# Kernel optimization log

Hardware: AMD Instinct MI355X
Metric: run time of the kernel (lower is better)

Reference implementation:

```python
import jax, jax.numpy as jnp
import numpy as np

GROUP = 32  # values per quantization group (per-group scale)

def setup_inputs() -> dict:
    key = jax.random.key(0)
    k1, k2, k3, k4 = jax.random.split(key, 4)
    B, S, IN, OUT = 4, 2048, 4096, 4096
    x = jax.random.normal(k1, (B, S, IN), dtype=jnp.float32)
    # packed 4-bit weights: each int32 byte-value in [0,256) holds two nibbles
    w_packed = jax.random.randint(k2, (OUT, IN // 2), 0, 256, dtype=jnp.int32)
    scales = jax.random.uniform(k3, (OUT, IN // GROUP), dtype=jnp.float32) * 0.02 + 0.001
    bias = jax.random.normal(k4, (OUT,), dtype=jnp.float32)
    return {"x": x, "w_packed": w_packed, "scales": scales, "bias": bias}

def _dequantize(w_packed, scales):
    # w_packed: [OUT, IN//2] int32 bytes, scales: [OUT, IN//GROUP]
    OUT = w_packed.shape[0]
    low = w_packed & 0xF
    high = (w_packed >> 4) & 0xF
    q = jnp.stack([low, high], axis=-1).reshape(OUT, -1)  # [OUT, IN]
    qf = q.astype(jnp.float32) - 8.0  # signed 4-bit centered at 8
    qg = qf.reshape(OUT, scales.shape[1], GROUP)
    w = qg * scales[:, :, None]
    return w.reshape(OUT, -1)  # [OUT, IN]

def reference(x, w_packed, scales, bias):
    # dequantize weights then F.linear: y = x @ W^T + b
    W = _dequantize(w_packed, scales)  # [OUT, IN]
    y = jnp.einsum('bsi,oi->bso', x, W) + bias
    return y
```

## Files before the change

kernel.cpp:

```cpp
#include <hip/hip_runtime.h>
#include <stdint.h>

#define M_TOT 8192
#define K_TOT 4096
#define N_TOT 4096
#define GROUPQ 32

#define BM 256
#define BN 256
#define BK 64
#define NT (K_TOT / BK)

typedef __bf16 bf16x8 __attribute__((ext_vector_type(8)));
typedef float f32x4 __attribute__((ext_vector_type(4)));
typedef unsigned short u16;
typedef unsigned short u16x8 __attribute__((ext_vector_type(8)));

__device__ __forceinline__ u16 f2bf_rne(float f) {
  union { float f; uint32_t u; } v; v.f = f;
  uint32_t u = v.u;
  uint32_t r = (u + 0x7FFFu + ((u >> 16) & 1u)) >> 16;
  return (u16)r;
}

__global__ void cvt_x_kernel(const float* __restrict__ x, u16* __restrict__ xb, int n8) {
  int stride = gridDim.x * blockDim.x;
  for (int i = blockIdx.x * blockDim.x + threadIdx.x; i < n8; i += stride) {
    const float4* p = (const float4*)(x + (size_t)i * 8);
    float4 a = p[0];
    float4 b = p[1];
    u16x8 o;
    o[0] = f2bf_rne(a.x); o[1] = f2bf_rne(a.y); o[2] = f2bf_rne(a.z); o[3] = f2bf_rne(a.w);
    o[4] = f2bf_rne(b.x); o[5] = f2bf_rne(b.y); o[6] = f2bf_rne(b.z); o[7] = f2bf_rne(b.w);
    *(u16x8*)(xb + (size_t)i * 8) = o;
  }
}

__global__ void dequant_w_kernel(const int* __restrict__ wp, const float* __restrict__ sc,
                                 u16* __restrict__ wb) {
  const int KH = K_TOT / 2;
  const int total = N_TOT * KH / 8;
  int stride = gridDim.x * blockDim.x;
  for (int t = blockIdx.x * blockDim.x + threadIdx.x; t < total; t += stride) {
    int base = t * 8;
    int o = base >> 11;
    int ci = base & 2047;
    int e0 = ci * 2;
    float scale = sc[o * (K_TOT / GROUPQ) + (e0 >> 5)];
    int4 p0 = *(const int4*)(wp + base);
    int4 p1 = *(const int4*)(wp + base + 4);
    int v[8] = {p0.x, p0.y, p0.z, p0.w, p1.x, p1.y, p1.z, p1.w};
    u16x8 oA, oB;
#pragma unroll
    for (int j = 0; j < 8; ++j) {
      float lo = (float)((v[j] & 0xF) - 8) * scale;
      float hi = (float)(((v[j] >> 4) & 0xF) - 8) * scale;
      u16 lob = f2bf_rne(lo), hib = f2bf_rne(hi);
      if (j < 4) { oA[2 * j] = lob; oA[2 * j + 1] = hib; }
      else       { oB[2 * (j - 4)] = lob; oB[2 * (j - 4) + 1] = hib; }
    }
    u16* dst = wb + (size_t)o * K_TOT + e0;
    *(u16x8*)dst = oA;
    *(u16x8*)(dst + 8) = oB;
  }
}

__global__ __launch_bounds__(512, 2) void gemm_bf16_kernel(
    const u16* __restrict__ A, const u16* __restrict__ Bt,
    const float* __restrict__ bias, float* __restrict__ C) {
  __shared__ alignas(16) u16 sL[65536];

  const int ntn = N_TOT / BN;
  int wg = blockIdx.x, nwg = gridDim.x;
  int cpx = nwg >> 3;
  int swz = (wg & 7) * cpx + (wg >> 3);
  int bm = swz / ntn, bn = swz % ntn;

  int tid = threadIdx.x, wid = tid >> 6, lane = tid & 63;
  int wr = wid >> 2, wc = wid & 3;
  const size_t K = K_TOT;

  int rowS = tid >> 2;
  int cgS = (tid & 3) ^ ((rowS >> 1) & 3);
  const u16* pA = A + ((size_t)(bm * 256 + (rowS >> 6) * 128 + (rowS & 63))) * K + cgS * 8;
  const u16* pB = Bt + ((size_t)(bn * 256 + (rowS >> 5) * 64 + (rowS & 31))) * K + cgS * 8;
  u16* sE = &sL[0];

  auto stA = [&](int T, int mh) {
    int buf = T & 1;
    const u16* s = pA + (size_t)mh * 64 * K + T * 64;
    u16* d0 = sE + ((buf * 2 + 0) * 2 + mh) * 4096 + tid * 8;
    u16* d1 = sE + ((buf * 2 + 1) * 2 + mh) * 4096 + tid * 8;
    __builtin_amdgcn_global_load_lds(
        (const __attribute__((address_space(1))) uint32_t*)s,
        (__attribute__((address_space(3))) uint32_t*)d0, 16, 0, 0);
    __builtin_amdgcn_global_load_lds(
        (const __attribute__((address_space(1))) uint32_t*)(s + 32),
        (__attribute__((address_space(3))) uint32_t*)d1, 16, 0, 0);
  };
  auto stB = [&](int T, int nh) {
    int buf = T & 1;
    const u16* s = pB + (size_t)nh * 32 * K + T * 64;
    u16* d0 = sE + 32768 + ((buf * 2 + 0) * 2 + nh) * 4096 + tid * 8;
    u16* d1 = sE + 32768 + ((buf * 2 + 1) * 2 + nh) * 4096 + tid * 8;
    __builtin_amdgcn_global_load_lds(
        (const __attribute__((address_space(1))) uint32_t*)s,
        (__attribute__((address_space(3))) uint32_t*)d0, 16, 0, 0);
    __builtin_amdgcn_global_load_lds(
        (const __attribute__((address_space(1))) uint32_t*)(s + 32),
        (__attribute__((address_space(3))) uint32_t*)d1, 16, 0, 0);
  };

  int rA = wr * 64 + (lane & 15);
  int cA = ((lane >> 4) ^ ((rA >> 1) & 3)) * 8;
  int rB = wc * 32 + (lane & 15);
  int cB = ((lane >> 4) ^ ((rB >> 1) & 3)) * 8;
  auto ldA = [&](int buf, int kk, int mh, int m3) {
    return *(const bf16x8*)(sE + ((buf * 2 + kk) * 2 + mh) * 4096 + (rA + m3 * 16) * 32 + cA);
  };
  auto ldB = [&](int buf, int kk, int nh, int n2) {
    return *(const bf16x8*)(sE + 32768 + ((buf * 2 + kk) * 2 + nh) * 4096 + (rB + n2 * 16) * 32 + cB);
  };

  f32x4 acc[8][4] = {};
  bf16x8 a0[4][2], a1[4][2], b0[2][2], b1[2][2];

  stA(0, 0); stB(0, 0); stB(0, 1); stA(0, 1);
  stA(1, 0); stB(1, 0); stB(1, 1); stA(1, 1);
  asm volatile("s_waitcnt vmcnt(4)" ::: "memory");
  __builtin_amdgcn_s_barrier();

#pragma unroll
  for (int m3 = 0; m3 < 4; ++m3)
#pragma unroll
    for (int kk = 0; kk < 2; ++kk) a0[m3][kk] = ldA(0, kk, 0, m3);
#pragma unroll
  for (int n2 = 0; n2 < 2; ++n2)
#pragma unroll
    for (int kk = 0; kk < 2; ++kk) b0[n2][kk] = ldB(0, kk, 0, n2);
  asm volatile("s_waitcnt lgkmcnt(0)" ::: "memory");
  __builtin_amdgcn_s_barrier();

  for (int t = 0; t < NT; ++t) {
    int buf = t & 1;
    int nbuf = buf ^ 1;
    bool st_ok = (t + 2 < NT);
    bool rd_ok = (t + 1 < NT);
    int Ts = t + 2;

#pragma unroll
    for (int n2 = 0; n2 < 2; ++n2)
#pragma unroll
      for (int kk = 0; kk < 2; ++kk) b1[n2][kk] = ldB(buf, kk, 1, n2);
    if (st_ok) stA(Ts, 0);
    __builtin_amdgcn_s_setprio(1);
#pragma unroll
    for (int kk = 0; kk < 2; ++kk)
#pragma unroll
      for (int m3 = 0; m3 < 4; ++m3)
#pragma unroll
        for (int n2 = 0; n2 < 2; ++n2)
          acc[m3][n2] = __builtin_amdgcn_mfma_f32_16x16x32_bf16(a0[m3][kk], b0[n2][kk], acc[m3][n2], 0, 0, 0);
    __builtin_amdgcn_s_setprio(0);

#pragma unroll
    for (int m3 = 0; m3 < 4; ++m3)
#pragma unroll
      for (int kk = 0; kk < 2; ++kk) a1[m3][kk] = ldA(buf, kk, 1, m3);
    if (st_ok) stB(Ts, 0);
    __builtin_amdgcn_s_setprio(1);
#pragma unroll
    for (int kk = 0; kk < 2; ++kk)
#pragma unroll
      for (int m3 = 0; m3 < 4; ++m3)
#pragma unroll
        for (int n2 = 0; n2 < 2; ++n2)
          acc[m3][n2 + 2] = __builtin_amdgcn_mfma_f32_16x16x32_bf16(a0[m3][kk], b1[n2][kk], acc[m3][n2 + 2], 0, 0, 0);
    __builtin_amdgcn_s_setprio(0);
    __builtin_amdgcn_s_barrier();

    if (rd_ok) {
#pragma unroll
      for (int m3 = 0; m3 < 4; ++m3)
#pragma unroll
        for (int kk = 0; kk < 2; ++kk) a0[m3][kk] = ldA(nbuf, kk, 0, m3);
    }
    if (st_ok) stB(Ts, 1);
    __builtin_amdgcn_s_setprio(1);
#pragma unroll
    for (int kk = 0; kk < 2; ++kk)
#pragma unroll
      for (int m3 = 0; m3 < 4; ++m3)
#pragma unroll
        for (int n2 = 0; n2 < 2; ++n2)
          acc[m3 + 4][n2] = __builtin_amdgcn_mfma_f32_16x16x32_bf16(a1[m3][kk], b0[n2][kk], acc[m3 + 4][n2], 0, 0, 0);
    __builtin_amdgcn_s_setprio(0);
    __builtin_amdgcn_s_barrier();

    if (rd_ok) {
#pragma unroll
      for (int n2 = 0; n2 < 2; ++n2)
#pragma unroll
        for (int kk = 0; kk < 2; ++kk) b0[n2][kk] = ldB(nbuf, kk, 0, n2);
    }
    if (st_ok) stA(Ts, 1);
    __builtin_amdgcn_s_setprio(1);
#pragma unroll
    for (int kk = 0; kk < 2; ++kk)
#pragma unroll
      for (int m3 = 0; m3 < 4; ++m3)
#pragma unroll
        for (int n2 = 0; n2 < 2; ++n2)
          acc[m3 + 4][n2 + 2] = __builtin_amdgcn_mfma_f32_16x16x32_bf16(a1[m3][kk], b1[n2][kk], acc[m3 + 4][n2 + 2], 0, 0, 0);
    __builtin_amdgcn_s_setprio(0);
    asm volatile("s_waitcnt lgkmcnt(0)" ::: "memory");
    if (t < NT - 2) { asm volatile("s_waitcnt vmcnt(4)" ::: "memory"); }
    else            { asm volatile("s_waitcnt vmcnt(0)" ::: "memory"); }
    __builtin_amdgcn_s_barrier();
  }

  asm volatile("s_waitcnt vmcnt(0)" ::: "memory");

  int col = lane & 15;
  int rb = (lane >> 4) * 4;
#pragma unroll
  for (int n = 0; n < 4; ++n) {
    int gn = bn * BN + wc * 64 + n * 16 + col;
    float bsv = bias[gn];
#pragma unroll
    for (int m = 0; m < 8; ++m) {
      int gm = bm * BM + wr * 128 + m * 16 + rb;
#pragma unroll
      for (int j = 0; j < 4; ++j)
        C[(size_t)(gm + j) * N_TOT + gn] = acc[m][n][j] + bsv;
    }
  }
}

__global__ void fill_kernel(float* p, int n, float v) {
  int stride = gridDim.x * blockDim.x;
  for (int i = blockIdx.x * blockDim.x + threadIdx.x; i < n; i += stride) p[i] = v;
}

extern "C" void kernel_launch(void* const* d_in, const int* in_sizes, int n_in,
                              void* d_out, int out_size, void* d_ws, size_t ws_size,
                              hipStream_t stream) {
  const float* x = (const float*)d_in[0];
  const int* wp = (const int*)d_in[1];
  const float* sc = (const float*)d_in[2];
  const float* bias = (const float*)d_in[3];
  float* out = (float*)d_out;

  size_t xb_bytes = (size_t)M_TOT * K_TOT * 2;
  size_t wb_bytes = (size_t)N_TOT * K_TOT * 2;
  if (ws_size < xb_bytes + wb_bytes) {
    fill_kernel<<<2048, 256, 0, stream>>>(out, out_size, 12345.0f);
    return;
  }
  u16* xb = (u16*)d_ws;
  u16* wb = (u16*)((char*)d_ws + xb_bytes);

  cvt_x_kernel<<<2048, 256, 0, stream>>>(x, xb, M_TOT * K_TOT / 8);
  dequant_w_kernel<<<2048, 256, 0, stream>>>(wp, sc, wb);
  gemm_bf16_kernel<<<(M_TOT / BM) * (N_TOT / BN), 512, 0, stream>>>(xb, wb, bias, out);
}
```

Before: 271.8 us.

## Triple-buffer second A/B halves in LDS to drop two per-iteration barriers

The second halves of the A and B tiles now get a three-stage LDS ring, while the first halves keep double buffering. Because of this, stores for the tile two steps ahead no longer overwrite data that other waves may still be reading, so two of the three block barriers per K iteration are removed. The aim is to cut synchronisation stalls between MFMA phases. LDS use per block grows from 128KB to 160KB, which may prevent two blocks from fitting on one CU as launch_bounds requests, and the mod-3 indexing adds some address arithmetic.

```diff
diff --git a/kernel.cpp b/kernel.cpp
--- a/kernel.cpp
+++ b/kernel.cpp
@@ -68,7 +68,8 @@
 __global__ __launch_bounds__(512, 2) void gemm_bf16_kernel(
     const u16* __restrict__ A, const u16* __restrict__ Bt,
     const float* __restrict__ bias, float* __restrict__ C) {
-  __shared__ alignas(16) u16 sL[65536];
+  __shared__ alignas(16) u16 sL[81920];
+  const int A0B = 0, B0B = 16384, A1B = 32768, B1B = 57344;
 
   const int ntn = N_TOT / BN;
   int wg = blockIdx.x, nwg = gridDim.x;
@@ -86,64 +87,76 @@
   const u16* pB = Bt + ((size_t)(bn * 256 + (rowS >> 5) * 64 + (rowS & 31))) * K + cgS * 8;
   u16* sE = &sL[0];
 
-  auto stA = [&](int T, int mh) {
+#define GLLDS(src, dst)                                                      \
+  __builtin_amdgcn_global_load_lds(                                          \
+      (const __attribute__((address_space(1))) uint32_t*)(src),              \
+      (__attribute__((address_space(3))) uint32_t*)(dst), 16, 0, 0)
+
+  auto stA0 = [&](int T) {
     int buf = T & 1;
-    const u16* s = pA + (size_t)mh * 64 * K + T * 64;
-    u16* d0 = sE + ((buf * 2 + 0) * 2 + mh) * 4096 + tid * 8;
-    u16* d1 = sE + ((buf * 2 + 1) * 2 + mh) * 4096 + tid * 8;
-    __builtin_amdgcn_global_load_lds(
-        (const __attribute__((address_space(1))) uint32_t*)s,
-        (__attribute__((address_space(3))) uint32_t*)d0, 16, 0, 0);
-    __builtin_amdgcn_global_load_lds(
-        (const __attribute__((address_space(1))) uint32_t*)(s + 32),
-        (__attribute__((address_space(3))) uint32_t*)d1, 16, 0, 0);
-  };
-  auto stB = [&](int T, int nh) {
+    const u16* s = pA + (size_t)T * 64;
+    GLLDS(s,      sE + A0B + (buf * 2 + 0) * 4096 + tid * 8);
+    GLLDS(s + 32, sE + A0B + (buf * 2 + 1) * 4096 + tid * 8);
+  };
+  auto stB0 = [&](int T) {
     int buf = T & 1;
-    const u16* s = pB + (size_t)nh * 32 * K + T * 64;
-    u16* d0 = sE + 32768 + ((buf * 2 + 0) * 2 + nh) * 4096 + tid * 8;
-    u16* d1 = sE + 32768 + ((buf * 2 + 1) * 2 + nh) * 4096 + tid * 8;
-    __builtin_amdgcn_global_load_lds(
-        (const __attribute__((address_space(1))) uint32_t*)s,
-        (__attribute__((address_space(3))) uint32_t*)d0, 16, 0, 0);
-    __builtin_amdgcn_global_load_lds(
-        (const __attribute__((address_space(1))) uint32_t*)(s + 32),
-        (__attribute__((address_space(3))) uint32_t*)d1, 16, 0, 0);
+    const u16* s = pB + (size_t)T * 64;
+    GLLDS(s,      sE + B0B + (buf * 2 + 0) * 4096 + tid * 8);
+    GLLDS(s + 32, sE + B0B + (buf * 2 + 1) * 4096 + tid * 8);
+  };
+  auto stA1 = [&](int T) {
+    int s3 = T % 3;
+    const u16* s = pA + (size_t)64 * K + (size_t)T * 64;
+    GLLDS(s,      sE + A1B + (s3 * 2 + 0) * 4096 + tid * 8);
+    GLLDS(s + 32, sE + A1B + (s3 * 2 + 1) * 4096 + tid * 8);
+  };
+  auto stB1 = [&](int T) {
+    int s3 = T % 3;
+    const u16* s = pB + (size_t)32 * K + (size_t)T * 64;
+    GLLDS(s,      sE + B1B + (s3 * 2 + 0) * 4096 + tid * 8);
+    GLLDS(s + 32, sE + B1B + (s3 * 2 + 1) * 4096 + tid * 8);
   };
 
   int rA = wr * 64 + (lane & 15);
   int cA = ((lane >> 4) ^ ((rA >> 1) & 3)) * 8;
   int rB = wc * 32 + (lane & 15);
   int cB = ((lane >> 4) ^ ((rB >> 1) & 3)) * 8;
-  auto ldA = [&](int buf, int kk, int mh, int m3) {
-    return *(const bf16x8*)(sE + ((buf * 2 + kk) * 2 + mh) * 4096 + (rA + m3 * 16) * 32 + cA);
-  };
-  auto ldB = [&](int buf, int kk, int nh, int n2) {
-    return *(const bf16x8*)(sE + 32768 + ((buf * 2 + kk) * 2 + nh) * 4096 + (rB + n2 * 16) * 32 + cB);
+  auto ldA0 = [&](int buf, int kk, int m3) {
+    return *(const bf16x8*)(sE + A0B + (buf * 2 + kk) * 4096 + (rA + m3 * 16) * 32 + cA);
+  };
+  auto ldA1 = [&](int s3, int kk, int m3) {
+    return *(const bf16x8*)(sE + A1B + (s3 * 2 + kk) * 4096 + (rA + m3 * 16) * 32 + cA);
+  };
+  auto ldB0 = [&](int buf, int kk, int n2) {
+    return *(const bf16x8*)(sE + B0B + (buf * 2 + kk) * 4096 + (rB + n2 * 16) * 32 + cB);
+  };
+  auto ldB1 = [&](int s3, int kk, int n2) {
+    return *(const bf16x8*)(sE + B1B + (s3 * 2 + kk) * 4096 + (rB + n2 * 16) * 32 + cB);
   };
 
   f32x4 acc[8][4] = {};
   bf16x8 a0[4][2], a1[4][2], b0[2][2], b1[2][2];
 
-  stA(0, 0); stB(0, 0); stB(0, 1); stA(0, 1);
-  stA(1, 0); stB(1, 0); stB(1, 1); stA(1, 1);
+  stA0(0); stB0(0); stA1(0); stB1(0);
+  stA0(1); stB0(1); stA1(1); stB1(1);
   asm volatile("s_waitcnt vmcnt(4)" ::: "memory");
   __builtin_amdgcn_s_barrier();
 
 #pragma unroll
   for (int m3 = 0; m3 < 4; ++m3)
 #pragma unroll
-    for (int kk = 0; kk < 2; ++kk) a0[m3][kk] = ldA(0, kk, 0, m3);
+    for (int kk = 0; kk < 2; ++kk) a0[m3][kk] = ldA0(0, kk, m3);
 #pragma unroll
   for (int n2 = 0; n2 < 2; ++n2)
 #pragma unroll
-    for (int kk = 0; kk < 2; ++kk) b0[n2][kk] = ldB(0, kk, 0, n2);
+    for (int kk = 0; kk < 2; ++kk) b0[n2][kk] = ldB0(0, kk, n2);
   asm volatile("s_waitcnt lgkmcnt(0)" ::: "memory");
   __builtin_amdgcn_s_barrier();
 
   for (int t = 0; t < NT; ++t) {
     int buf = t & 1;
     int nbuf = buf ^ 1;
+    int s3 = t % 3;
     bool st_ok = (t + 2 < NT);
     bool rd_ok = (t + 1 < NT);
     int Ts = t + 2;
@@ -151,8 +164,8 @@
 #pragma unroll
     for (int n2 = 0; n2 < 2; ++n2)
 #pragma unroll
-      for (int kk = 0; kk < 2; ++kk) b1[n2][kk] = ldB(buf, kk, 1, n2);
-    if (st_ok) stA(Ts, 0);
+      for (int kk = 0; kk < 2; ++kk) b1[n2][kk] = ldB1(s3, kk, n2);
+    if (st_ok) stA0(Ts);
     __builtin_amdgcn_s_setprio(1);
 #pragma unroll
     for (int kk = 0; kk < 2; ++kk)
@@ -166,8 +179,8 @@
 #pragma unroll
     for (int m3 = 0; m3 < 4; ++m3)
 #pragma unroll
-      for (int kk = 0; kk < 2; ++kk) a1[m3][kk] = ldA(buf, kk, 1, m3);
-    if (st_ok) stB(Ts, 0);
+      for (int kk = 0; kk < 2; ++kk) a1[m3][kk] = ldA1(s3, kk, m3);
+    if (st_ok) stB0(Ts);
     __builtin_amdgcn_s_setprio(1);
 #pragma unroll
     for (int kk = 0; kk < 2; ++kk)
@@ -177,15 +190,14 @@
         for (int n2 = 0; n2 < 2; ++n2)
           acc[m3][n2 + 2] = __builtin_amdgcn_mfma_f32_16x16x32_bf16(a0[m3][kk], b1[n2][kk], acc[m3][n2 + 2], 0, 0, 0);
     __builtin_amdgcn_s_setprio(0);
-    __builtin_amdgcn_s_barrier();
 
     if (rd_ok) {
 #pragma unroll
       for (int m3 = 0; m3 < 4; ++m3)
 #pragma unroll
-        for (int kk = 0; kk < 2; ++kk) a0[m3][kk] = ldA(nbuf, kk, 0, m3);
-    }
-    if (st_ok) stB(Ts, 1);
+        for (int kk = 0; kk < 2; ++kk) a0[m3][kk] = ldA0(nbuf, kk, m3);
+    }
+    if (st_ok) stA1(Ts);
     __builtin_amdgcn_s_setprio(1);
 #pragma unroll
     for (int kk = 0; kk < 2; ++kk)
@@ -195,15 +207,14 @@
         for (int n2 = 0; n2 < 2; ++n2)
           acc[m3 + 4][n2] = __builtin_amdgcn_mfma_f32_16x16x32_bf16(a1[m3][kk], b0[n2][kk], acc[m3 + 4][n2], 0, 0, 0);
     __builtin_amdgcn_s_setprio(0);
-    __builtin_amdgcn_s_barrier();
 
     if (rd_ok) {
 #pragma unroll
       for (int n2 = 0; n2 < 2; ++n2)
 #pragma unroll
-        for (int kk = 0; kk < 2; ++kk) b0[n2][kk] = ldB(nbuf, kk, 0, n2);
-    }
-    if (st_ok) stA(Ts, 1);
+        for (int kk = 0; kk < 2; ++kk) b0[n2][kk] = ldB0(nbuf, kk, n2);
+    }
+    if (st_ok) stB1(Ts);
     __builtin_amdgcn_s_setprio(1);
 #pragma unroll
     for (int kk = 0; kk < 2; ++kk)
@@ -235,6 +246,7 @@
         C[(size_t)(gm + j) * N_TOT + gn] = acc[m][n][j] + bsv;
     }
   }
+#undef GLLDS
 }
 
 __global__ void fill_kernel(float* p, int n, float v) {
```

Result: no change. 273.5 us (+0.6%).
